# Kernel optimization log

Hardware: AMD Instinct MI355X
Metric: run time of the kernel (lower is better)

Reference implementation:

```python
import jax, jax.numpy as jnp
import numpy as np

D_IN = 1024
D_OUT = 1024
SEQ = 2048
BATCH = 4


def setup_inputs() -> dict:
    key = jax.random.key(0)
    k_x, k_q, k_k, k_v = jax.random.split(key, 4)
    scale = 1.0 / np.sqrt(D_IN)  # ~ torch Linear init scale
    x = jax.random.normal(k_x, (BATCH, SEQ, D_IN), dtype=jnp.float32)
    # torch nn.Linear weights have shape [d_out, d_in]; y = x @ W.T
    Wq = jax.random.uniform(k_q, (D_OUT, D_IN), jnp.float32, -scale, scale)
    Wk = jax.random.uniform(k_k, (D_OUT, D_IN), jnp.float32, -scale, scale)
    Wv = jax.random.uniform(k_v, (D_OUT, D_IN), jnp.float32, -scale, scale)
    return {"x": x, "Wq": Wq, "Wk": Wk, "Wv": Wv}


def reference(x, Wq, Wk, Wv):
    # projections (no bias, qkv_bias=False)
    q = jnp.einsum("bsd,ed->bse", x, Wq)  # [B,S,D_OUT]
    k = jnp.einsum("bsd,ed->bse", x, Wk)
    v = jnp.einsum("bsd,ed->bse", x, Wv)
    scores = jnp.einsum("bqe,bke->bqk", q, k)  # [B,S,S]
    seq = scores.shape[-1]
    causal = jnp.tril(jnp.ones((seq, seq), dtype=bool))  # keep lower-tri
    scores = jnp.where(causal[None], scores, -jnp.inf)
    # note: original scales AFTER masking: softmax(scores / sqrt(d_k))
    inv_sqrt_dk = 1.0 / np.sqrt(k.shape[-1]).astype(np.float32)
    weights = jax.nn.softmax(scores * inv_sqrt_dk, axis=-1)
    # dropout p=0.0 (eval-equivalent): identity
    return jnp.einsum("bqk,bke->bqe", weights, v)
```

## Files before the change

### kernel.cpp

```cpp
#include <hip/hip_runtime.h>
#include <hip/hip_bf16.h>

typedef __bf16 v8bf __attribute__((ext_vector_type(8)));
typedef float v4f __attribute__((ext_vector_type(4)));

#define GBL_AS(p) ((const __attribute__((address_space(1))) unsigned int*)(p))
#define LDS_AS(p) ((__attribute__((address_space(3))) unsigned int*)(p))

#define WAIT_VM4() __builtin_amdgcn_s_waitcnt(0x0F74)
#define WAIT_VM0() __builtin_amdgcn_s_waitcnt(0x0F70)

__global__ void cast_f32_bf16(const float* __restrict__ src,
                              __hip_bfloat16* __restrict__ dst, int n) {
  int i = (blockIdx.x * 256 + threadIdx.x) * 4;
  if (i >= n) return;
  float4 f = *(const float4*)(src + i);
  union { __hip_bfloat16 h[4]; uint2 u; } pk;
  pk.h[0] = __float2bfloat16(f.x);
  pk.h[1] = __float2bfloat16(f.y);
  pk.h[2] = __float2bfloat16(f.z);
  pk.h[3] = __float2bfloat16(f.w);
  *(uint2*)(dst + i) = pk.u;
}

__global__ void cast_w3(const float* __restrict__ a, const float* __restrict__ b,
                        const float* __restrict__ c, __hip_bfloat16* __restrict__ dst) {
  int seg = blockIdx.x >> 10;
  const float* src = seg == 0 ? a : (seg == 1 ? b : c);
  int i = ((blockIdx.x & 1023) * 256 + threadIdx.x) * 4;
  float4 f = *(const float4*)(src + i);
  union { __hip_bfloat16 h[4]; uint2 u; } pk;
  pk.h[0] = __float2bfloat16(f.x);
  pk.h[1] = __float2bfloat16(f.y);
  pk.h[2] = __float2bfloat16(f.z);
  pk.h[3] = __float2bfloat16(f.w);
  *(uint2*)(dst + seg * 1048576 + i) = pk.u;
}

__global__ void transpose_bf16(const __hip_bfloat16* __restrict__ src,
                               __hip_bfloat16* __restrict__ dst,
                               int rows, int cols) {
  __shared__ __hip_bfloat16 t[32][33];
  long boff = (long)blockIdx.z * rows * cols;
  src += boff; dst += boff;
  int c0 = blockIdx.x * 32, r0 = blockIdx.y * 32;
  int x = threadIdx.x;
#pragma unroll
  for (int i = 0; i < 4; ++i) {
    int y = threadIdx.y + i * 8;
    t[y][x] = src[(long)(r0 + y) * cols + (c0 + x)];
  }
  __syncthreads();
#pragma unroll
  for (int i = 0; i < 4; ++i) {
    int y = threadIdx.y + i * 8;
    dst[(long)(c0 + y) * rows + (r0 + x)] = t[x][y];
  }
}

template<int MODE>
__global__ __launch_bounds__(256, 4)
void gemm_nt(const __hip_bfloat16* __restrict__ A, long sAb, int lda,
             const __hip_bfloat16* __restrict__ B, long sBb, int ldb,
             void* __restrict__ Cv, long sCb, int ldc,
             int K, float scale, float* __restrict__ sums) {
  const int tid = threadIdx.x;
  const int l = tid & 63, w = tid >> 6;
  int z, nb, mb, kend = K;
  if (MODE == 0) {
    z = blockIdx.x >> 3; nb = (blockIdx.x & 7) << 7; mb = blockIdx.y << 7;
  } else if (MODE == 1) {
    const int id = blockIdx.x;
    z = id & 3;
    const int t = id >> 2;
    int m = (int)((__builtin_sqrtf(8.0f * t + 1.0f) - 1.0f) * 0.5f);
    while ((m + 1) * (m + 2) / 2 <= t) ++m;
    while (m * (m + 1) / 2 > t) --m;
    mb = m << 7;
    nb = (t - m * (m + 1) / 2) << 7;
  } else {
    const int id = blockIdx.x;
    const int half = id >> 8, r8 = id & 255;
    const int m = r8 >> 4, low = r8 & 15;
    nb = (low >> 1) << 7;
    z = (half << 1) | (low & 1);
    const int mi = half ? (15 - m) : m;
    mb = mi << 7;
    kend = (mi + 1) << 7;
  }

  A += (long)z * sAb;
  B += (long)z * sBb;

  __shared__ alignas(16) __hip_bfloat16 As[3][128 * 32];
  __shared__ alignas(16) __hip_bfloat16 Bs[3][128 * 32];

  v4f acc[4][4] = {};
  const int wm = (w >> 1) * 64, wn = (w & 1) * 64;

  const int cb0 = w * 64;
  const int row0s = (cb0 + l) >> 2, col0s = ((cb0 + l) & 3) << 3;
  const int cb1 = 256 + w * 64;
  const int row1s = (cb1 + l) >> 2, col1s = ((cb1 + l) & 3) << 3;

  const __hip_bfloat16* Arow0 = A + (long)(mb + row0s) * lda + col0s;
  const __hip_bfloat16* Arow1 = A + (long)(mb + row1s) * lda + col1s;
  const __hip_bfloat16* Brow0 = B + (long)(nb + row0s) * ldb + col0s;
  const __hip_bfloat16* Brow1 = B + (long)(nb + row1s) * ldb + col1s;

  auto stage = [&](int k0, int buf) {
    __builtin_amdgcn_global_load_lds(GBL_AS(Arow0 + k0),
        LDS_AS(&As[buf][cb0 * 8]), 16, 0, 0);
    __builtin_amdgcn_global_load_lds(GBL_AS(Brow0 + k0),
        LDS_AS(&Bs[buf][cb0 * 8]), 16, 0, 0);
    __builtin_amdgcn_global_load_lds(GBL_AS(Arow1 + k0),
        LDS_AS(&As[buf][cb1 * 8]), 16, 0, 0);
    __builtin_amdgcn_global_load_lds(GBL_AS(Brow1 + k0),
        LDS_AS(&Bs[buf][cb1 * 8]), 16, 0, 0);
  };

  stage(0, 0);
  if (32 < kend) stage(32, 1);

  int bi = 0;
  for (int k0 = 0; k0 < kend; k0 += 32) {
    if (k0 + 32 < kend) WAIT_VM4(); else WAIT_VM0();
    __builtin_amdgcn_s_barrier();
    if (k0 + 64 < kend) stage(k0 + 64, bi == 0 ? 2 : bi - 1);

    v8bf af[4], bfr[4];
#pragma unroll
    for (int i = 0; i < 4; ++i) {
      af[i]  = *(const v8bf*)(&As[bi][(wm + i * 16 + (l & 15)) * 32 + ((l >> 4) << 3)]);
      bfr[i] = *(const v8bf*)(&Bs[bi][(wn + i * 16 + (l & 15)) * 32 + ((l >> 4) << 3)]);
    }
#pragma unroll
    for (int i = 0; i < 4; ++i)
#pragma unroll
      for (int j = 0; j < 4; ++j)
        acc[i][j] = __builtin_amdgcn_mfma_f32_16x16x32_bf16(af[i], bfr[j], acc[i][j], 0, 0, 0);
    bi = (bi == 2) ? 0 : bi + 1;
  }

  const int col0 = nb + wn + (l & 15);
  const int row0 = mb + wm + ((l >> 4) << 2);
  if constexpr (MODE == 0) {
    __hip_bfloat16* C = (__hip_bfloat16*)Cv + (long)z * sCb;
#pragma unroll
    for (int i = 0; i < 4; ++i)
#pragma unroll
      for (int r = 0; r < 4; ++r) {
        long ro = (long)(row0 + i * 16 + r) * ldc;
#pragma unroll
        for (int j = 0; j < 4; ++j)
          C[ro + col0 + j * 16] = __float2bfloat16(acc[i][j][r] * scale);
      }
  } else if constexpr (MODE == 1) {
    __hip_bfloat16* C = (__hip_bfloat16*)Cv + (long)z * sCb;
    float* srow = sums + z * 2048;
#pragma unroll
    for (int i = 0; i < 4; ++i)
#pragma unroll
      for (int r = 0; r < 4; ++r) {
        const int m = row0 + i * 16 + r;
        long ro = (long)m * ldc;
        float sp = 0.f;
#pragma unroll
        for (int j = 0; j < 4; ++j) {
          const int n = col0 + j * 16;
          float p = (n <= m) ? __expf(acc[i][j][r] * scale) : 0.0f;
          sp += p;
          C[ro + n] = __float2bfloat16(p);
        }
        sp += __shfl_xor(sp, 1);
        sp += __shfl_xor(sp, 2);
        sp += __shfl_xor(sp, 4);
        sp += __shfl_xor(sp, 8);
        if ((l & 15) == 0) atomicAdd(&srow[m], sp);
      }
  } else {
    float* C = (float*)Cv + (long)z * sCb;
    const float* srow = sums + z * 2048;
#pragma unroll
    for (int i = 0; i < 4; ++i)
#pragma unroll
      for (int r = 0; r < 4; ++r) {
        const int m = row0 + i * 16 + r;
        const float s = 1.0f / srow[m];
        long ro = (long)m * ldc;
#pragma unroll
        for (int j = 0; j < 4; ++j)
          C[ro + col0 + j * 16] = acc[i][j][r] * s;
      }
  }
}

extern "C" void kernel_launch(void* const* d_in, const int* in_sizes, int n_in,
                              void* d_out, int out_size, void* d_ws, size_t ws_size,
                              hipStream_t stream) {
  const float* x  = (const float*)d_in[0];
  const float* Wq = (const float*)d_in[1];
  const float* Wk = (const float*)d_in[2];
  const float* Wv = (const float*)d_in[3];
  float* out = (float*)d_out;
  char* ws = (char*)d_ws;

  __hip_bfloat16* qkv = (__hip_bfloat16*)ws;
  __hip_bfloat16* vT  = (__hip_bfloat16*)(ws + 50331648);
  __hip_bfloat16* xb  = (__hip_bfloat16*)(ws + 67108864);
  __hip_bfloat16* Wb  = (__hip_bfloat16*)(ws + 83886080);
  __hip_bfloat16* P   = (__hip_bfloat16*)(ws + 67108864);
  float* sums         = (float*)(ws + 100663296);

  hipMemsetAsync(sums, 0, 8192 * sizeof(float), stream);

  cast_f32_bf16<<<8192, 256, 0, stream>>>(x, xb, 8388608);
  cast_w3<<<3072, 256, 0, stream>>>(Wq, Wk, Wv, Wb);

  gemm_nt<0><<<dim3(24, 64, 1), 256, 0, stream>>>(
      xb, 0L, 1024, Wb, 1048576L, 1024, qkv, 8388608L, 1024,
      1024, 1.0f, nullptr);

  transpose_bf16<<<dim3(32, 64, 4), dim3(32, 8), 0, stream>>>(
      qkv + 16777216, vT, 2048, 1024);

  gemm_nt<1><<<dim3(544, 1, 1), 256, 0, stream>>>(
      qkv, 2097152L, 1024, qkv + 8388608, 2097152L, 1024,
      P, 4194304L, 2048, 1024, 0.03125f, sums);

  gemm_nt<2><<<dim3(512, 1, 1), 256, 0, stream>>>(
      P, 4194304L, 2048, vT, 2097152L, 2048,
      out, 2097152L, 1024, 2048, 1.0f, sums);
}
```

Baseline: 246.6 us.

## Fuse V transpose into projection GEMM epilogue and fully unroll fixed-K loop

The separate transpose kernel is removed. The projection GEMM now writes the V output directly in transposed layout from its epilogue, with each lane packing 4 consecutive rows into one 8-byte store. The K loop for modes 0 and 1 is fully unrolled via macros with a K of 1024 hard-coded, and launch bounds drop from 4 to 3 waves per SIMD. This removes a kernel launch and a full read/write pass over V, at the cost of strided transposed stores, larger code, and a hard-coded K assumption.

New measurement: 235.4 us. -4.5%, faster.

```diff
diff --git a/kernel.cpp b/kernel.cpp
--- a/kernel.cpp
+++ b/kernel.cpp
@@ -37,33 +37,13 @@
   *(uint2*)(dst + seg * 1048576 + i) = pk.u;
 }
 
-__global__ void transpose_bf16(const __hip_bfloat16* __restrict__ src,
-                               __hip_bfloat16* __restrict__ dst,
-                               int rows, int cols) {
-  __shared__ __hip_bfloat16 t[32][33];
-  long boff = (long)blockIdx.z * rows * cols;
-  src += boff; dst += boff;
-  int c0 = blockIdx.x * 32, r0 = blockIdx.y * 32;
-  int x = threadIdx.x;
-#pragma unroll
-  for (int i = 0; i < 4; ++i) {
-    int y = threadIdx.y + i * 8;
-    t[y][x] = src[(long)(r0 + y) * cols + (c0 + x)];
-  }
-  __syncthreads();
-#pragma unroll
-  for (int i = 0; i < 4; ++i) {
-    int y = threadIdx.y + i * 8;
-    dst[(long)(c0 + y) * rows + (r0 + x)] = t[x][y];
-  }
-}
-
 template<int MODE>
-__global__ __launch_bounds__(256, 4)
+__global__ __launch_bounds__(256, 3)
 void gemm_nt(const __hip_bfloat16* __restrict__ A, long sAb, int lda,
              const __hip_bfloat16* __restrict__ B, long sBb, int ldb,
              void* __restrict__ Cv, long sCb, int ldc,
-             int K, float scale, float* __restrict__ sums) {
+             int K, float scale, float* __restrict__ sums,
+             __hip_bfloat16* __restrict__ vTp) {
   const int tid = threadIdx.x;
   const int l = tid & 63, w = tid >> 6;
   int z, nb, mb, kend = K;
@@ -108,53 +88,114 @@
   const __hip_bfloat16* Brow0 = B + (long)(nb + row0s) * ldb + col0s;
   const __hip_bfloat16* Brow1 = B + (long)(nb + row1s) * ldb + col1s;
 
-  auto stage = [&](int k0, int buf) {
-    __builtin_amdgcn_global_load_lds(GBL_AS(Arow0 + k0),
-        LDS_AS(&As[buf][cb0 * 8]), 16, 0, 0);
-    __builtin_amdgcn_global_load_lds(GBL_AS(Brow0 + k0),
-        LDS_AS(&Bs[buf][cb0 * 8]), 16, 0, 0);
-    __builtin_amdgcn_global_load_lds(GBL_AS(Arow1 + k0),
-        LDS_AS(&As[buf][cb1 * 8]), 16, 0, 0);
-    __builtin_amdgcn_global_load_lds(GBL_AS(Brow1 + k0),
-        LDS_AS(&Bs[buf][cb1 * 8]), 16, 0, 0);
-  };
-
-  stage(0, 0);
-  if (32 < kend) stage(32, 1);
-
-  int bi = 0;
-  for (int k0 = 0; k0 < kend; k0 += 32) {
-    if (k0 + 32 < kend) WAIT_VM4(); else WAIT_VM0();
-    __builtin_amdgcn_s_barrier();
-    if (k0 + 64 < kend) stage(k0 + 64, bi == 0 ? 2 : bi - 1);
-
-    v8bf af[4], bfr[4];
-#pragma unroll
-    for (int i = 0; i < 4; ++i) {
-      af[i]  = *(const v8bf*)(&As[bi][(wm + i * 16 + (l & 15)) * 32 + ((l >> 4) << 3)]);
-      bfr[i] = *(const v8bf*)(&Bs[bi][(wn + i * 16 + (l & 15)) * 32 + ((l >> 4) << 3)]);
+  const int ldsA = (wm + (l & 15)) * 32 + ((l >> 4) << 3);
+  const int ldsB = (wn + (l & 15)) * 32 + ((l >> 4) << 3);
+
+#define STAGE_T(K0, BUF) do {                                                   \
+    __builtin_amdgcn_global_load_lds(GBL_AS(Arow0 + (K0)),                      \
+        LDS_AS(&As[BUF][cb0 * 8]), 16, 0, 0);                                   \
+    __builtin_amdgcn_global_load_lds(GBL_AS(Brow0 + (K0)),                      \
+        LDS_AS(&Bs[BUF][cb0 * 8]), 16, 0, 0);                                   \
+    __builtin_amdgcn_global_load_lds(GBL_AS(Arow1 + (K0)),                      \
+        LDS_AS(&As[BUF][cb1 * 8]), 16, 0, 0);                                   \
+    __builtin_amdgcn_global_load_lds(GBL_AS(Brow1 + (K0)),                      \
+        LDS_AS(&Bs[BUF][cb1 * 8]), 16, 0, 0);                                   \
+  } while (0)
+
+#define COMPUTE(BI) do {                                                        \
+    v8bf af[4], bfr[4];                                                         \
+    _Pragma("unroll")                                                           \
+    for (int i = 0; i < 4; ++i) {                                               \
+      af[i]  = *(const v8bf*)(&As[BI][ldsA + i * 512]);                         \
+      bfr[i] = *(const v8bf*)(&Bs[BI][ldsB + i * 512]);                         \
+    }                                                                           \
+    _Pragma("unroll")                                                           \
+    for (int i = 0; i < 4; ++i)                                                 \
+      _Pragma("unroll")                                                         \
+      for (int j = 0; j < 4; ++j)                                               \
+        acc[i][j] = __builtin_amdgcn_mfma_f32_16x16x32_bf16(af[i], bfr[j],      \
+                                                            acc[i][j], 0, 0, 0);\
+  } while (0)
+
+#define KITER(IT) do {                                                          \
+    if constexpr ((IT) < 31) WAIT_VM4(); else WAIT_VM0();                       \
+    __builtin_amdgcn_s_barrier();                                               \
+    if constexpr ((IT) < 30) STAGE_T((IT) * 32 + 64, ((IT) + 2) % 3);           \
+    COMPUTE((IT) % 3);                                                          \
+  } while (0)
+
+  if constexpr (MODE == 0 || MODE == 1) {
+    STAGE_T(0, 0);
+    STAGE_T(32, 1);
+    KITER(0);  KITER(1);  KITER(2);  KITER(3);  KITER(4);  KITER(5);  KITER(6);
+    KITER(7);  KITER(8);  KITER(9);  KITER(10); KITER(11); KITER(12); KITER(13);
+    KITER(14); KITER(15); KITER(16); KITER(17); KITER(18); KITER(19); KITER(20);
+    KITER(21); KITER(22); KITER(23); KITER(24); KITER(25); KITER(26); KITER(27);
+    KITER(28); KITER(29); KITER(30); KITER(31);
+  } else {
+    auto stage = [&](int k0, int buf) {
+      __builtin_amdgcn_global_load_lds(GBL_AS(Arow0 + k0),
+          LDS_AS(&As[buf][cb0 * 8]), 16, 0, 0);
+      __builtin_amdgcn_global_load_lds(GBL_AS(Brow0 + k0),
+          LDS_AS(&Bs[buf][cb0 * 8]), 16, 0, 0);
+      __builtin_amdgcn_global_load_lds(GBL_AS(Arow1 + k0),
+          LDS_AS(&As[buf][cb1 * 8]), 16, 0, 0);
+      __builtin_amdgcn_global_load_lds(GBL_AS(Brow1 + k0),
+          LDS_AS(&Bs[buf][cb1 * 8]), 16, 0, 0);
+    };
+    stage(0, 0);
+    if (32 < kend) stage(32, 1);
+    int bi = 0;
+    for (int k0 = 0; k0 < kend; k0 += 32) {
+      if (k0 + 32 < kend) WAIT_VM4(); else WAIT_VM0();
+      __builtin_amdgcn_s_barrier();
+      if (k0 + 64 < kend) stage(k0 + 64, bi == 0 ? 2 : bi - 1);
+      v8bf af[4], bfr[4];
+#pragma unroll
+      for (int i = 0; i < 4; ++i) {
+        af[i]  = *(const v8bf*)(&As[bi][ldsA + i * 512]);
+        bfr[i] = *(const v8bf*)(&Bs[bi][ldsB + i * 512]);
+      }
+#pragma unroll
+      for (int i = 0; i < 4; ++i)
+#pragma unroll
+        for (int j = 0; j < 4; ++j)
+          acc[i][j] = __builtin_amdgcn_mfma_f32_16x16x32_bf16(af[i], bfr[j], acc[i][j], 0, 0, 0);
+      bi = (bi == 2) ? 0 : bi + 1;
     }
-#pragma unroll
-    for (int i = 0; i < 4; ++i)
-#pragma unroll
-      for (int j = 0; j < 4; ++j)
-        acc[i][j] = __builtin_amdgcn_mfma_f32_16x16x32_bf16(af[i], bfr[j], acc[i][j], 0, 0, 0);
-    bi = (bi == 2) ? 0 : bi + 1;
   }
+#undef KITER
+#undef COMPUTE
+#undef STAGE_T
 
   const int col0 = nb + wn + (l & 15);
   const int row0 = mb + wm + ((l >> 4) << 2);
   if constexpr (MODE == 0) {
-    __hip_bfloat16* C = (__hip_bfloat16*)Cv + (long)z * sCb;
-#pragma unroll
-    for (int i = 0; i < 4; ++i)
-#pragma unroll
-      for (int r = 0; r < 4; ++r) {
-        long ro = (long)(row0 + i * 16 + r) * ldc;
-#pragma unroll
-        for (int j = 0; j < 4; ++j)
-          C[ro + col0 + j * 16] = __float2bfloat16(acc[i][j][r] * scale);
-      }
+    if (z < 2) {
+      __hip_bfloat16* C = (__hip_bfloat16*)Cv + (long)z * sCb;
+#pragma unroll
+      for (int i = 0; i < 4; ++i)
+#pragma unroll
+        for (int r = 0; r < 4; ++r) {
+          long ro = (long)(row0 + i * 16 + r) * ldc;
+#pragma unroll
+          for (int j = 0; j < 4; ++j)
+            C[ro + col0 + j * 16] = __float2bfloat16(acc[i][j][r] * scale);
+        }
+    } else {
+      const long b = row0 >> 11;
+      const int seq0 = row0 & 2047;
+#pragma unroll
+      for (int i = 0; i < 4; ++i)
+#pragma unroll
+        for (int j = 0; j < 4; ++j) {
+          union { __hip_bfloat16 h[4]; uint2 u; } pk;
+#pragma unroll
+          for (int r = 0; r < 4; ++r) pk.h[r] = __float2bfloat16(acc[i][j][r]);
+          *(uint2*)(vTp + b * 2097152 + (long)(col0 + j * 16) * 2048 +
+                    (seq0 + i * 16)) = pk.u;
+        }
+    }
   } else if constexpr (MODE == 1) {
     __hip_bfloat16* C = (__hip_bfloat16*)Cv + (long)z * sCb;
     float* srow = sums + z * 2048;
@@ -219,16 +260,13 @@
 
   gemm_nt<0><<<dim3(24, 64, 1), 256, 0, stream>>>(
       xb, 0L, 1024, Wb, 1048576L, 1024, qkv, 8388608L, 1024,
-      1024, 1.0f, nullptr);
-
-  transpose_bf16<<<dim3(32, 64, 4), dim3(32, 8), 0, stream>>>(
-      qkv + 16777216, vT, 2048, 1024);
+      1024, 1.0f, nullptr, vT);
 
   gemm_nt<1><<<dim3(544, 1, 1), 256, 0, stream>>>(
       qkv, 2097152L, 1024, qkv + 8388608, 2097152L, 1024,
-      P, 4194304L, 2048, 1024, 0.03125f, sums);
+      P, 4194304L, 2048, 1024, 0.03125f, sums, nullptr);
 
   gemm_nt<2><<<dim3(512, 1, 1), 256, 0, stream>>>(
       P, 4194304L, 2048, vT, 2097152L, 2048,
-      out, 2097152L, 1024, 2048, 1.0f, sums);
-}
+      out, 2097152L, 1024, 2048, 1.0f, sums, nullptr);
+}
```
